# Kernel optimization log

Measured on AMD Instinct MI355X. Metric: run time of the kernel, lower is better.

## Reference

```python
import jax, jax.numpy as jnp
import numpy as np

N_NODES = 50000
N_EDGES = 800000
IN_CH = 64
HID_CH = 128
LAT_CH = 64
N_GRAPHS = 64
U_DIM = 32


def setup_inputs() -> dict:
    key = jax.random.key(0)
    ks = jax.random.split(key, 12)
    x = jax.random.normal(ks[0], (N_NODES, IN_CH), dtype=jnp.float32)
    edge_index = jax.random.randint(ks[1], (2, N_EDGES), 0, N_NODES, dtype=jnp.int64)
    edge_attr = jax.random.normal(ks[2], (N_EDGES, 8), dtype=jnp.float32)  # unused by NodeModel
    u = jax.random.normal(ks[3], (N_GRAPHS, U_DIM), dtype=jnp.float32)
    batch = jnp.sort(jax.random.randint(ks[4], (N_NODES,), 0, N_GRAPHS, dtype=jnp.int64))
    s = 0.02
    W1 = jax.random.normal(ks[5], (2 * IN_CH, HID_CH), dtype=jnp.float32) * s
    b1 = jnp.zeros((HID_CH,), dtype=jnp.float32)
    W2 = jax.random.normal(ks[6], (HID_CH, HID_CH), dtype=jnp.float32) * s
    b2 = jnp.zeros((HID_CH,), dtype=jnp.float32)
    W3 = jax.random.normal(ks[7], (HID_CH, LAT_CH), dtype=jnp.float32) * s
    b3 = jnp.zeros((LAT_CH,), dtype=jnp.float32)
    return {"x": x, "edge_index": edge_index, "edge_attr": edge_attr, "u": u,
            "batch": batch, "W1": W1, "b1": b1, "W2": W2, "b2": b2, "W3": W3, "b3": b3}


def reference(x, edge_index, edge_attr, u, batch, W1, b1, W2, b2, W3, b3):
    row, col = edge_index[0], edge_index[1]
    # gather endpoints -> [E, 2*in_ch]
    h = jnp.concatenate([x[row], x[col]], axis=1)
    # 3-layer MLP on edges
    h = jax.nn.relu(h @ W1 + b1)
    h = jax.nn.relu(h @ W2 + b2)
    h = h @ W3 + b3  # [E, latent]
    # scatter reductions over destination node (col)
    cnt = jax.ops.segment_sum(jnp.ones((h.shape[0],), h.dtype), col, num_segments=N_NODES)
    mean = jax.ops.segment_sum(h, col, num_segments=N_NODES) / jnp.maximum(cnt, 1.0)[:, None]
    mx = jax.ops.segment_max(h, col, num_segments=N_NODES)
    mn = jax.ops.segment_min(h, col, num_segments=N_NODES)
    nonempty = (cnt > 0)[:, None]
    mx = jnp.where(nonempty, mx, 0.0)  # torch_scatter returns 0 for empty segments
    mn = jnp.where(nonempty, mn, 0.0)
    return jnp.concatenate([x, mean, mx, mn, u[batch]], axis=1)
```

## Files before the change

kernel.cpp:

```cpp
#include <hip/hip_runtime.h>

#define E_EDGES 800000
#define NN 50000
#define OUT_STRIDE 288

typedef __bf16 bf16;
typedef bf16 bf16x8 __attribute__((ext_vector_type(8)));
typedef float floatx4 __attribute__((ext_vector_type(4)));
typedef float floatx2 __attribute__((ext_vector_type(2)));
typedef unsigned short ushort8v __attribute__((ext_vector_type(8)));

__device__ __forceinline__ unsigned short f2bf(float f){
    return __builtin_bit_cast(unsigned short, (bf16)f);
}
__device__ __forceinline__ unsigned pack2bf(float a, float b){
    unsigned short lo = __builtin_bit_cast(unsigned short, (bf16)a);
    unsigned short hi = __builtin_bit_cast(unsigned short, (bf16)b);
    return (unsigned)lo | ((unsigned)hi << 16);
}
__device__ __forceinline__ float bf2f(unsigned short h){
    return __uint_as_float((unsigned)h << 16);
}
__device__ __forceinline__ unsigned encf(float f){
    unsigned u = __float_as_uint(f);
    return (u & 0x80000000u) ? ~u : (u | 0x80000000u);
}
__device__ __forceinline__ float decf(unsigned u){
    return __uint_as_float((u & 0x80000000u) ? (u ^ 0x80000000u) : ~u);
}
__device__ __forceinline__ floatx4 mfma16(ushort8v a, ushort8v b, floatx4 c){
    return __builtin_amdgcn_mfma_f32_16x16x32_bf16(
        __builtin_bit_cast(bf16x8, a), __builtin_bit_cast(bf16x8, b), c, 0, 0, 0);
}
__device__ __forceinline__ void flush_run(float* out, int node, float s, float mx, float mn, int lane){
    float* sp = out + (long)node * OUT_STRIDE + 64;
    atomicAdd(sp + lane, s);
    atomicMax((unsigned*)sp + 64 + lane, encf(mx));
    atomicMin((unsigned*)sp + 128 + lane, encf(mn));
}
__device__ __forceinline__ ushort8v combine_relu_pq(ushort8v p, uint2 q){
    floatx2 q01 = __builtin_amdgcn_cvt_pk_f32_fp8((int)q.x, false);
    floatx2 q23 = __builtin_amdgcn_cvt_pk_f32_fp8((int)q.x, true);
    floatx2 q45 = __builtin_amdgcn_cvt_pk_f32_fp8((int)q.y, false);
    floatx2 q67 = __builtin_amdgcn_cvt_pk_f32_fp8((int)q.y, true);
    uint4 o;
    o.x = pack2bf(fmaxf(bf2f(p[0]) + q01[0], 0.f), fmaxf(bf2f(p[1]) + q01[1], 0.f));
    o.y = pack2bf(fmaxf(bf2f(p[2]) + q23[0], 0.f), fmaxf(bf2f(p[3]) + q23[1], 0.f));
    o.z = pack2bf(fmaxf(bf2f(p[4]) + q45[0], 0.f), fmaxf(bf2f(p[5]) + q45[1], 0.f));
    o.w = pack2bf(fmaxf(bf2f(p[6]) + q67[0], 0.f), fmaxf(bf2f(p[7]) + q67[1], 0.f));
    return __builtin_bit_cast(ushort8v, o);
}

#define INIT_N 2400000
#define PK_N   40960
#define SETUP_TOTAL (INIT_N + PK_N + E_EDGES)

__global__ void setup_kernel(const int* __restrict__ ei,
                             const float* __restrict__ W1, const float* __restrict__ W2,
                             const float* __restrict__ W3,
                             unsigned short* __restrict__ wp,
                             int* __restrict__ cnt, float* __restrict__ out)
{
    int i = blockIdx.x * blockDim.x + threadIdx.x;
    if (i < INIT_N) {
        int row = i / 48, q = i % 48;
        uint4 val = (q < 32) ? make_uint4(0u, 0u, 0u, 0u)
                             : make_uint4(~0u, ~0u, ~0u, ~0u);
        ((uint4*)out)[(long)row * 72 + 16 + q] = val;
        return;
    }
    i -= INIT_N;
    if (i < PK_N) {
        const float* W; int N; int idx;
        if (i < 16384)      { W = W1; N = 128; idx = i; }
        else if (i < 32768) { W = W2; N = 128; idx = i - 16384; }
        else                { W = W3; N = 64;  idx = i - 32768; }
        int j = idx & 7, lane = (idx >> 3) & 63, kc = (idx >> 9) & 3, nt = idx >> 11;
        wp[i] = f2bf(W[(kc * 32 + ((lane >> 4) & 3) * 8 + j) * N + nt * 16 + (lane & 15)]);
        return;
    }
    i -= PK_N;
    if (i < E_EDGES) atomicAdd(&cnt[ei[E_EDGES + i]], 1);
}

#define PQ_BLOCKS 391
__global__ __launch_bounds__(256, 4) void pq_kernel(
    const float* __restrict__ x, const unsigned short* __restrict__ wp,
    const float* __restrict__ b1, float* __restrict__ out, unsigned char* __restrict__ qb)
{
    const int tid = threadIdx.x, lane = tid & 63, w = tid >> 6;
    const int quad = lane >> 4, ln = lane & 15;
    const ushort8v* wpv = (const ushort8v*)wp;
    const int nbase = (blockIdx.x * 4 + w) * 32;
    const int n0 = nbase + ln, n1 = nbase + 16 + ln;
    const int n0c = min(n0, NN - 1), n1c = min(n1, NN - 1);

    ushort8v X0[2], X1[2];
#pragma unroll
    for (int c = 0; c < 2; c++){
        const float4* p0 = (const float4*)(x + (long)n0c * 64 + c * 32 + quad * 8);
        const float4* p1 = (const float4*)(x + (long)n1c * 64 + c * 32 + quad * 8);
        float4 a = p0[0], b = p0[1];
        float4 cc = p1[0], d = p1[1];
        uint4 u0, u1;
        u0.x = pack2bf(a.x, a.y);  u0.y = pack2bf(a.z, a.w);
        u0.z = pack2bf(b.x, b.y);  u0.w = pack2bf(b.z, b.w);
        u1.x = pack2bf(cc.x, cc.y); u1.y = pack2bf(cc.z, cc.w);
        u1.z = pack2bf(d.x, d.y);  u1.w = pack2bf(d.z, d.w);
        X0[c] = __builtin_bit_cast(ushort8v, u0);
        X1[c] = __builtin_bit_cast(ushort8v, u1);
    }
    unsigned char* ob = (unsigned char*)out;
#pragma unroll
    for (int nt = 0; nt < 8; nt++){
        floatx4 bini = *(const floatx4*)(b1 + nt * 16 + quad * 4);
        floatx4 z = {0.f, 0.f, 0.f, 0.f};
        floatx4 aP0 = bini, aP1 = bini, aQ0 = z, aQ1 = z;
        ushort8v Af0 = wpv[(nt * 4 + 0) * 64 + lane];
        ushort8v Af1 = wpv[(nt * 4 + 1) * 64 + lane];
        ushort8v Af2 = wpv[(nt * 4 + 2) * 64 + lane];
        ushort8v Af3 = wpv[(nt * 4 + 3) * 64 + lane];
        aP0 = mfma16(Af0, X0[0], aP0); aP0 = mfma16(Af1, X0[1], aP0);
        aP1 = mfma16(Af0, X1[0], aP1); aP1 = mfma16(Af1, X1[1], aP1);
        aQ0 = mfma16(Af2, X0[0], aQ0); aQ0 = mfma16(Af3, X0[1], aQ0);
        aQ1 = mfma16(Af2, X1[0], aQ1); aQ1 = mfma16(Af3, X1[1], aQ1);
        uint2 sP0, sP1;
        sP0.x = pack2bf(aP0[0], aP0[1]); sP0.y = pack2bf(aP0[2], aP0[3]);
        sP1.x = pack2bf(aP1[0], aP1[1]); sP1.y = pack2bf(aP1[2], aP1[3]);
        int bo = nt * 32 + quad * 8;
        int q0p = __builtin_amdgcn_cvt_pk_fp8_f32(aQ0[0], aQ0[1], 0, false);
        q0p     = __builtin_amdgcn_cvt_pk_fp8_f32(aQ0[2], aQ0[3], q0p, true);
        int q1p = __builtin_amdgcn_cvt_pk_fp8_f32(aQ1[0], aQ1[1], 0, false);
        q1p     = __builtin_amdgcn_cvt_pk_fp8_f32(aQ1[2], aQ1[3], q1p, true);
        int qo = nt * 16 + quad * 4;
        if (n0 < NN){
            *(uint2*)(ob + (long)n0 * 1152 + bo) = sP0;
            *(int*)(qb + (long)n0 * 128 + qo)    = q0p;
        }
        if (n1 < NN){
            *(uint2*)(ob + (long)n1 * 1152 + bo) = sP1;
            *(int*)(qb + (long)n1 * 128 + qo)    = q1p;
        }
    }
}

__global__ void scanA_kernel(const int* __restrict__ cnt, int* __restrict__ off,
                             int* __restrict__ bsum){
    __shared__ int s[256];
    int tid = threadIdx.x;
    int node = blockIdx.x * 196 + tid;
    int val = (tid < 196 && node < NN) ? cnt[node] : 0;
    s[tid] = val;
    __syncthreads();
    for (int d = 1; d < 256; d <<= 1){
        int t = (tid >= d) ? s[tid - d] : 0;
        __syncthreads();
        s[tid] += t;
        __syncthreads();
    }
    if (tid < 196 && node < NN) off[node] = s[tid] - val;
    if (tid == 255) bsum[blockIdx.x] = s[255];
}

__global__ void scanB_kernel(const int* __restrict__ bsum, int* __restrict__ bbase){
    __shared__ int s[256];
    int tid = threadIdx.x;
    int val = bsum[tid];
    s[tid] = val;
    __syncthreads();
    for (int d = 1; d < 256; d <<= 1){
        int t = (tid >= d) ? s[tid - d] : 0;
        __syncthreads();
        s[tid] += t;
        __syncthreads();
    }
    bbase[tid] = s[tid] - val;
}

__global__ void scatter_kernel(const int* __restrict__ ei, int* __restrict__ off,
                               const int* __restrict__ bbase, int2* __restrict__ enodes){
    int e = blockIdx.x * blockDim.x + threadIdx.x;
    if (e >= E_EDGES) return;
    int c = ei[E_EDGES + e], r = ei[e];
    int pos = atomicAdd(&off[c], 1) + bbase[c / 196];
    enodes[pos] = make_int2(r, c);
}

__global__ __launch_bounds__(256, 5) void edge_mlp_kernel(
    const int2* __restrict__ enodes, const unsigned short* __restrict__ wp,
    const unsigned char* __restrict__ qb,
    const float* __restrict__ b2, const float* __restrict__ b3,
    float* __restrict__ out)
{
    __shared__ __align__(16) unsigned char smem[4 * 4608];

    const int tid  = threadIdx.x;
    const int lane = tid & 63;
    const int w    = tid >> 6;
    const int quad = lane >> 4;
    const int ln   = lane & 15;
    unsigned short* wbuf = (unsigned short*)(smem + w * 4608);
    float* Tf = (float*)wbuf;
    const ushort8v* wpv = (const ushort8v*)wp;

    const int g = blockIdx.x * 4 + w;
    const int ebase = g * 32;
    int2 ed0 = enodes[ebase + ln];
    int2 ed1 = enodes[ebase + 16 + ln];
    const int cn0 = ed0.y, cn1 = ed1.y;

    const unsigned short* pqb = (const unsigned short*)out;
    ushort8v H0[4], H1[4];
#pragma unroll
    for (int kc = 0; kc < 4; kc++){
        const int o = kc * 32 + quad * 8;
        ushort8v p0 = *(const ushort8v*)(pqb + (long)ed0.x * 576 + o);
        ushort8v p1 = *(const ushort8v*)(pqb + (long)ed1.x * 576 + o);
        uint2 q0 = *(const uint2*)(qb + (long)ed0.y * 128 + o);
        uint2 q1 = *(const uint2*)(qb + (long)ed1.y * 128 + o);
        H0[kc] = combine_relu_pq(p0, q0);
        H1[kc] = combine_relu_pq(p1, q1);
    }

    ushort8v G0[4], G1[4];
#pragma unroll
    for (int hv = 0; hv < 2; hv++){
#pragma unroll
        for (int q2 = 0; q2 < 4; q2++){
            int nt = hv * 4 + q2;
            floatx4 bini = *(const floatx4*)(b2 + nt * 16 + quad * 4);
            floatx4 a0 = bini, a1 = bini;
#pragma unroll
            for (int kc = 0; kc < 4; kc++){
                ushort8v Af = wpv[2048 + (nt * 4 + kc) * 64 + lane];
                a0 = mfma16(Af, H0[kc], a0);
                a1 = mfma16(Af, H1[kc], a1);
            }
            uint2 p0, p1;
            p0.x = pack2bf(fmaxf(a0[0], 0.f), fmaxf(a0[1], 0.f));
            p0.y = pack2bf(fmaxf(a0[2], 0.f), fmaxf(a0[3], 0.f));
            p1.x = pack2bf(fmaxf(a1[0], 0.f), fmaxf(a1[1], 0.f));
            p1.y = pack2bf(fmaxf(a1[2], 0.f), fmaxf(a1[3], 0.f));
            int col = q2 * 16 + quad * 4;
            *(uint2*)(wbuf + ln * 72 + col)        = p0;
            *(uint2*)(wbuf + (16 + ln) * 72 + col) = p1;
        }
#pragma unroll
        for (int c = 0; c < 2; c++){
            G0[hv * 2 + c] = *(const ushort8v*)(wbuf + ln * 72 + c * 32 + quad * 8);
            G1[hv * 2 + c] = *(const ushort8v*)(wbuf + (16 + ln) * 72 + c * 32 + quad * 8);
        }
    }

#pragma unroll
    for (int hv = 0; hv < 2; hv++){
#pragma unroll
        for (int q3 = 0; q3 < 2; q3++){
            int nt = hv * 2 + q3;
            floatx4 bini = *(const floatx4*)(b3 + nt * 16 + quad * 4);
            floatx4 a0 = bini, a1 = bini;
#pragma unroll
            for (int kc = 0; kc < 4; kc++){
                ushort8v Af = wpv[4096 + (nt * 4 + kc) * 64 + lane];
                a0 = mfma16(Af, G0[kc], a0);
                a1 = mfma16(Af, G1[kc], a1);
            }
            int row = q3 * 16 + quad * 4;
#pragma unroll
            for (int r = 0; r < 4; r++){
                Tf[(row + r) * 36 + ln]      = a0[r];
                Tf[(row + r) * 36 + 16 + ln] = a1[r];
            }
        }
        if ((lane >> 5) == hv){
            float v[32];
#pragma unroll
            for (int jj = 0; jj < 8; jj++){
                floatx4 t = *(const floatx4*)(Tf + (lane & 31) * 36 + jj * 4);
                v[jj * 4 + 0] = t[0]; v[jj * 4 + 1] = t[1];
                v[jj * 4 + 2] = t[2]; v[jj * 4 + 3] = t[3];
            }
            int cur = __builtin_amdgcn_readlane(cn0, 0);
            float s = v[0], mx = v[0], mn = v[0];
#pragma unroll
            for (int j = 1; j < 32; j++){
                int nj = (j < 16) ? __builtin_amdgcn_readlane(cn0, j)
                                  : __builtin_amdgcn_readlane(cn1, j - 16);
                if (nj != cur){
                    flush_run(out, cur, s, mx, mn, lane);
                    cur = nj; s = v[j]; mx = v[j]; mn = v[j];
                } else {
                    s += v[j]; mx = fmaxf(mx, v[j]); mn = fminf(mn, v[j]);
                }
            }
            flush_run(out, cur, s, mx, mn, lane);
        }
    }
}

__global__ void finalize_kernel(const float* __restrict__ x, const float* __restrict__ u,
                                const int* __restrict__ batch, const int* __restrict__ cnt,
                                float* __restrict__ out)
{
    long i = (long)blockIdx.x * blockDim.x + threadIdx.x;
    if (i >= (long)NN * 72) return;
    int ndx = (int)(i / 72);
    int q   = (int)(i % 72);
    float4 res;
    if (q < 16) {
        res = ((const float4*)(x + (long)ndx * 64))[q];
    } else if (q < 32) {
        float4 sv = ((const float4*)out)[i];
        int k = cnt[ndx];
        float inv = 1.f / (float)(k > 0 ? k : 1);
        res.x = sv.x * inv; res.y = sv.y * inv; res.z = sv.z * inv; res.w = sv.w * inv;
    } else if (q < 64) {
        uint4 e = ((const uint4*)out)[i];
        bool ne = cnt[ndx] > 0;
        res.x = ne ? decf(e.x) : 0.f; res.y = ne ? decf(e.y) : 0.f;
        res.z = ne ? decf(e.z) : 0.f; res.w = ne ? decf(e.w) : 0.f;
    } else {
        res = ((const float4*)(u + (long)batch[ndx] * 32))[q - 64];
    }
    ((float4*)out)[i] = res;
}

extern "C" void kernel_launch(void* const* d_in, const int* in_sizes, int n_in,
                              void* d_out, int out_size, void* d_ws, size_t ws_size,
                              hipStream_t stream)
{
    const float* x     = (const float*)d_in[0];
    const int*   ei    = (const int*)d_in[1];
    const float* u     = (const float*)d_in[3];
    const int*   batch = (const int*)d_in[4];
    const float* W1    = (const float*)d_in[5];
    const float* b1    = (const float*)d_in[6];
    const float* W2    = (const float*)d_in[7];
    const float* b2    = (const float*)d_in[8];
    const float* W3    = (const float*)d_in[9];
    const float* b3    = (const float*)d_in[10];
    float* out = (float*)d_out;
    unsigned char* ws = (unsigned char*)d_ws;

    unsigned short* wp     = (unsigned short*)ws;
    int*            cnt    = (int*)(ws + 81920);
    int*            off    = (int*)(ws + 281920);
    int*            bsum   = (int*)(ws + 481920);
    int*            bbase  = (int*)(ws + 482944);
    int2*           enodes = (int2*)(ws + 483968);
    unsigned char*  qb     = (unsigned char*)(ws + 6883968);

    hipMemsetAsync(cnt, 0, 200000, stream);
    setup_kernel<<<(SETUP_TOTAL + 255) / 256, 256, 0, stream>>>(ei, W1, W2, W3, wp, cnt, out);
    pq_kernel<<<PQ_BLOCKS, 256, 0, stream>>>(x, wp, b1, out, qb);
    scanA_kernel<<<256, 256, 0, stream>>>(cnt, off, bsum);
    scanB_kernel<<<1, 256, 0, stream>>>(bsum, bbase);
    scatter_kernel<<<(E_EDGES + 255) / 256, 256, 0, stream>>>(ei, off, bbase, enodes);
    edge_mlp_kernel<<<6250, 256, 0, stream>>>(enodes, wp, qb, b2, b3, out);
    finalize_kernel<<<(int)(((long)NN * 72 + 255) / 256), 256, 0, stream>>>(x, u, batch, cnt, out);
}
```

Measured before the change: 363.9 us.

## Store P table in fp8, pack edge indices, restructure layer-3 reduction

The first-layer source-node projection P is now stored as fp8 in a separate 128-byte-per-node buffer instead of bf16 inside the output tensor, with a permuted layout so each lane loads its 32 bytes in two 16-byte reads. Edge endpoints are packed into one 32-bit word (16-bit row and column), which halves the size of the sorted edge list. The layer-3 result is staged in LDS as bf16, and all 64 lanes each reduce one channel over both 16-edge halves, instead of two half-wave passes through a float staging buffer. Occupancy bounds rise from 5 to 8 blocks. The aim is less gather bandwidth and fewer serial reduction passes, at the cost of extra fp8 and bf16 rounding error, and the 16-bit packing only holds while node indices fit in 16 bits.

Result: no change. 361.9 us (-0.6%).

```diff
diff --git a/kernel.cpp b/kernel.cpp
--- a/kernel.cpp
+++ b/kernel.cpp
@@ -18,9 +18,6 @@
     unsigned short hi = __builtin_bit_cast(unsigned short, (bf16)b);
     return (unsigned)lo | ((unsigned)hi << 16);
 }
-__device__ __forceinline__ float bf2f(unsigned short h){
-    return __uint_as_float((unsigned)h << 16);
-}
 __device__ __forceinline__ unsigned encf(float f){
     unsigned u = __float_as_uint(f);
     return (u & 0x80000000u) ? ~u : (u | 0x80000000u);
@@ -38,16 +35,21 @@
     atomicMax((unsigned*)sp + 64 + lane, encf(mx));
     atomicMin((unsigned*)sp + 128 + lane, encf(mn));
 }
-__device__ __forceinline__ ushort8v combine_relu_pq(ushort8v p, uint2 q){
+__device__ __forceinline__ ushort8v combine_relu_fp8(uint2 p, uint2 q){
+    floatx2 p01 = __builtin_amdgcn_cvt_pk_f32_fp8((int)p.x, false);
+    floatx2 p23 = __builtin_amdgcn_cvt_pk_f32_fp8((int)p.x, true);
+    floatx2 p45 = __builtin_amdgcn_cvt_pk_f32_fp8((int)p.y, false);
+    floatx2 p67 = __builtin_amdgcn_cvt_pk_f32_fp8((int)p.y, true);
     floatx2 q01 = __builtin_amdgcn_cvt_pk_f32_fp8((int)q.x, false);
     floatx2 q23 = __builtin_amdgcn_cvt_pk_f32_fp8((int)q.x, true);
     floatx2 q45 = __builtin_amdgcn_cvt_pk_f32_fp8((int)q.y, false);
     floatx2 q67 = __builtin_amdgcn_cvt_pk_f32_fp8((int)q.y, true);
+    floatx2 s01 = p01 + q01, s23 = p23 + q23, s45 = p45 + q45, s67 = p67 + q67;
     uint4 o;
-    o.x = pack2bf(fmaxf(bf2f(p[0]) + q01[0], 0.f), fmaxf(bf2f(p[1]) + q01[1], 0.f));
-    o.y = pack2bf(fmaxf(bf2f(p[2]) + q23[0], 0.f), fmaxf(bf2f(p[3]) + q23[1], 0.f));
-    o.z = pack2bf(fmaxf(bf2f(p[4]) + q45[0], 0.f), fmaxf(bf2f(p[5]) + q45[1], 0.f));
-    o.w = pack2bf(fmaxf(bf2f(p[6]) + q67[0], 0.f), fmaxf(bf2f(p[7]) + q67[1], 0.f));
+    o.x = pack2bf(fmaxf(s01[0], 0.f), fmaxf(s01[1], 0.f));
+    o.y = pack2bf(fmaxf(s23[0], 0.f), fmaxf(s23[1], 0.f));
+    o.z = pack2bf(fmaxf(s45[0], 0.f), fmaxf(s45[1], 0.f));
+    o.w = pack2bf(fmaxf(s67[0], 0.f), fmaxf(s67[1], 0.f));
     return __builtin_bit_cast(ushort8v, o);
 }
 
@@ -86,7 +88,8 @@
 #define PQ_BLOCKS 391
 __global__ __launch_bounds__(256, 4) void pq_kernel(
     const float* __restrict__ x, const unsigned short* __restrict__ wp,
-    const float* __restrict__ b1, float* __restrict__ out, unsigned char* __restrict__ qb)
+    const float* __restrict__ b1,
+    unsigned char* __restrict__ pb, unsigned char* __restrict__ qb)
 {
     const int tid = threadIdx.x, lane = tid & 63, w = tid >> 6;
     const int quad = lane >> 4, ln = lane & 15;
@@ -110,7 +113,6 @@
         X0[c] = __builtin_bit_cast(ushort8v, u0);
         X1[c] = __builtin_bit_cast(ushort8v, u1);
     }
-    unsigned char* ob = (unsigned char*)out;
 #pragma unroll
     for (int nt = 0; nt < 8; nt++){
         floatx4 bini = *(const floatx4*)(b1 + nt * 16 + quad * 4);
@@ -124,22 +126,22 @@
         aP1 = mfma16(Af0, X1[0], aP1); aP1 = mfma16(Af1, X1[1], aP1);
         aQ0 = mfma16(Af2, X0[0], aQ0); aQ0 = mfma16(Af3, X0[1], aQ0);
         aQ1 = mfma16(Af2, X1[0], aQ1); aQ1 = mfma16(Af3, X1[1], aQ1);
-        uint2 sP0, sP1;
-        sP0.x = pack2bf(aP0[0], aP0[1]); sP0.y = pack2bf(aP0[2], aP0[3]);
-        sP1.x = pack2bf(aP1[0], aP1[1]); sP1.y = pack2bf(aP1[2], aP1[3]);
-        int bo = nt * 32 + quad * 8;
+        int p0p = __builtin_amdgcn_cvt_pk_fp8_f32(aP0[0], aP0[1], 0, false);
+        p0p     = __builtin_amdgcn_cvt_pk_fp8_f32(aP0[2], aP0[3], p0p, true);
+        int p1p = __builtin_amdgcn_cvt_pk_fp8_f32(aP1[0], aP1[1], 0, false);
+        p1p     = __builtin_amdgcn_cvt_pk_fp8_f32(aP1[2], aP1[3], p1p, true);
         int q0p = __builtin_amdgcn_cvt_pk_fp8_f32(aQ0[0], aQ0[1], 0, false);
         q0p     = __builtin_amdgcn_cvt_pk_fp8_f32(aQ0[2], aQ0[3], q0p, true);
         int q1p = __builtin_amdgcn_cvt_pk_fp8_f32(aQ1[0], aQ1[1], 0, false);
         q1p     = __builtin_amdgcn_cvt_pk_fp8_f32(aQ1[2], aQ1[3], q1p, true);
-        int qo = nt * 16 + quad * 4;
+        int g0 = ((nt & 1) * 2 + (quad >> 1)) * 32 + (nt >> 1) * 8 + (quad & 1) * 4;
         if (n0 < NN){
-            *(uint2*)(ob + (long)n0 * 1152 + bo) = sP0;
-            *(int*)(qb + (long)n0 * 128 + qo)    = q0p;
+            *(int*)(pb + (long)n0 * 128 + g0) = p0p;
+            *(int*)(qb + (long)n0 * 128 + g0) = q0p;
         }
         if (n1 < NN){
-            *(uint2*)(ob + (long)n1 * 1152 + bo) = sP1;
-            *(int*)(qb + (long)n1 * 128 + qo)    = q1p;
+            *(int*)(pb + (long)n1 * 128 + g0) = p1p;
+            *(int*)(qb + (long)n1 * 128 + g0) = q1p;
         }
     }
 }
@@ -178,48 +180,56 @@
 }
 
 __global__ void scatter_kernel(const int* __restrict__ ei, int* __restrict__ off,
-                               const int* __restrict__ bbase, int2* __restrict__ enodes){
+                               const int* __restrict__ bbase, unsigned* __restrict__ enodes){
     int e = blockIdx.x * blockDim.x + threadIdx.x;
     if (e >= E_EDGES) return;
     int c = ei[E_EDGES + e], r = ei[e];
     int pos = atomicAdd(&off[c], 1) + bbase[c / 196];
-    enodes[pos] = make_int2(r, c);
-}
-
-__global__ __launch_bounds__(256, 5) void edge_mlp_kernel(
-    const int2* __restrict__ enodes, const unsigned short* __restrict__ wp,
-    const unsigned char* __restrict__ qb,
+    enodes[pos] = (unsigned)r | ((unsigned)c << 16);
+}
+
+__global__ __launch_bounds__(256, 8) void edge_mlp_kernel(
+    const unsigned* __restrict__ enodes, const unsigned short* __restrict__ wp,
+    const unsigned char* __restrict__ pb, const unsigned char* __restrict__ qb,
     const float* __restrict__ b2, const float* __restrict__ b3,
     float* __restrict__ out)
 {
-    __shared__ __align__(16) unsigned char smem[4 * 4608];
+    __shared__ __align__(16) unsigned char smem[4 * 4864];
 
     const int tid  = threadIdx.x;
     const int lane = tid & 63;
     const int w    = tid >> 6;
     const int quad = lane >> 4;
     const int ln   = lane & 15;
-    unsigned short* wbuf = (unsigned short*)(smem + w * 4608);
-    float* Tf = (float*)wbuf;
+    unsigned short* wbuf = (unsigned short*)(smem + w * 4864);
     const ushort8v* wpv = (const ushort8v*)wp;
 
     const int g = blockIdx.x * 4 + w;
     const int ebase = g * 32;
-    int2 ed0 = enodes[ebase + ln];
-    int2 ed1 = enodes[ebase + 16 + ln];
-    const int cn0 = ed0.y, cn1 = ed1.y;
-
-    const unsigned short* pqb = (const unsigned short*)out;
+    unsigned e0 = enodes[ebase + ln];
+    unsigned e1 = enodes[ebase + 16 + ln];
+    const int r0 = (int)(e0 & 0xFFFFu), cn0 = (int)(e0 >> 16);
+    const int r1 = (int)(e1 & 0xFFFFu), cn1 = (int)(e1 >> 16);
+
     ushort8v H0[4], H1[4];
-#pragma unroll
-    for (int kc = 0; kc < 4; kc++){
-        const int o = kc * 32 + quad * 8;
-        ushort8v p0 = *(const ushort8v*)(pqb + (long)ed0.x * 576 + o);
-        ushort8v p1 = *(const ushort8v*)(pqb + (long)ed1.x * 576 + o);
-        uint2 q0 = *(const uint2*)(qb + (long)ed0.y * 128 + o);
-        uint2 q1 = *(const uint2*)(qb + (long)ed1.y * 128 + o);
-        H0[kc] = combine_relu_pq(p0, q0);
-        H1[kc] = combine_relu_pq(p1, q1);
+    {
+        const long po = (long)quad * 32;
+        uint4 pA = *(const uint4*)(pb + (long)r0  * 128 + po);
+        uint4 pB = *(const uint4*)(pb + (long)r0  * 128 + po + 16);
+        uint4 qA = *(const uint4*)(qb + (long)cn0 * 128 + po);
+        uint4 qB = *(const uint4*)(qb + (long)cn0 * 128 + po + 16);
+        uint4 rA = *(const uint4*)(pb + (long)r1  * 128 + po);
+        uint4 rB = *(const uint4*)(pb + (long)r1  * 128 + po + 16);
+        uint4 sA = *(const uint4*)(qb + (long)cn1 * 128 + po);
+        uint4 sB = *(const uint4*)(qb + (long)cn1 * 128 + po + 16);
+        H0[0] = combine_relu_fp8(make_uint2(pA.x, pA.y), make_uint2(qA.x, qA.y));
+        H0[1] = combine_relu_fp8(make_uint2(pA.z, pA.w), make_uint2(qA.z, qA.w));
+        H0[2] = combine_relu_fp8(make_uint2(pB.x, pB.y), make_uint2(qB.x, qB.y));
+        H0[3] = combine_relu_fp8(make_uint2(pB.z, pB.w), make_uint2(qB.z, qB.w));
+        H1[0] = combine_relu_fp8(make_uint2(rA.x, rA.y), make_uint2(sA.x, sA.y));
+        H1[1] = combine_relu_fp8(make_uint2(rA.z, rA.w), make_uint2(sA.z, sA.w));
+        H1[2] = combine_relu_fp8(make_uint2(rB.x, rB.y), make_uint2(sB.x, sB.y));
+        H1[3] = combine_relu_fp8(make_uint2(rB.z, rB.w), make_uint2(sB.z, sB.w));
     }
 
     ushort8v G0[4], G1[4];
@@ -253,49 +263,56 @@
     }
 
 #pragma unroll
-    for (int hv = 0; hv < 2; hv++){
-#pragma unroll
-        for (int q3 = 0; q3 < 2; q3++){
-            int nt = hv * 2 + q3;
-            floatx4 bini = *(const floatx4*)(b3 + nt * 16 + quad * 4);
-            floatx4 a0 = bini, a1 = bini;
-#pragma unroll
-            for (int kc = 0; kc < 4; kc++){
-                ushort8v Af = wpv[4096 + (nt * 4 + kc) * 64 + lane];
-                a0 = mfma16(Af, G0[kc], a0);
-                a1 = mfma16(Af, G1[kc], a1);
-            }
-            int row = q3 * 16 + quad * 4;
-#pragma unroll
-            for (int r = 0; r < 4; r++){
-                Tf[(row + r) * 36 + ln]      = a0[r];
-                Tf[(row + r) * 36 + 16 + ln] = a1[r];
-            }
-        }
-        if ((lane >> 5) == hv){
-            float v[32];
-#pragma unroll
-            for (int jj = 0; jj < 8; jj++){
-                floatx4 t = *(const floatx4*)(Tf + (lane & 31) * 36 + jj * 4);
-                v[jj * 4 + 0] = t[0]; v[jj * 4 + 1] = t[1];
-                v[jj * 4 + 2] = t[2]; v[jj * 4 + 3] = t[3];
-            }
-            int cur = __builtin_amdgcn_readlane(cn0, 0);
-            float s = v[0], mx = v[0], mn = v[0];
-#pragma unroll
-            for (int j = 1; j < 32; j++){
-                int nj = (j < 16) ? __builtin_amdgcn_readlane(cn0, j)
-                                  : __builtin_amdgcn_readlane(cn1, j - 16);
-                if (nj != cur){
-                    flush_run(out, cur, s, mx, mn, lane);
-                    cur = nj; s = v[j]; mx = v[j]; mn = v[j];
-                } else {
-                    s += v[j]; mx = fmaxf(mx, v[j]); mn = fminf(mn, v[j]);
-                }
-            }
-            flush_run(out, cur, s, mx, mn, lane);
-        }
-    }
+    for (int nt = 0; nt < 4; nt++){
+        floatx4 bini = *(const floatx4*)(b3 + nt * 16 + quad * 4);
+        floatx4 a0 = bini, a1 = bini;
+#pragma unroll
+        for (int kc = 0; kc < 4; kc++){
+            ushort8v Af = wpv[4096 + (nt * 4 + kc) * 64 + lane];
+            a0 = mfma16(Af, G0[kc], a0);
+            a1 = mfma16(Af, G1[kc], a1);
+        }
+        int och = nt * 16 + quad * 4;
+#pragma unroll
+        for (int r = 0; r < 4; r++){
+            wbuf[(och + r) * 38 + ln]      = f2bf(a0[r]);
+            wbuf[(och + r) * 38 + 16 + ln] = f2bf(a1[r]);
+        }
+    }
+
+    float v[32];
+#pragma unroll
+    for (int t = 0; t < 8; t++){
+        unsigned a = *(const unsigned*)(wbuf + lane * 38 + t * 4);
+        unsigned b = *(const unsigned*)(wbuf + lane * 38 + t * 4 + 2);
+        v[t * 4 + 0] = __uint_as_float(a << 16);
+        v[t * 4 + 1] = __uint_as_float(a & 0xFFFF0000u);
+        v[t * 4 + 2] = __uint_as_float(b << 16);
+        v[t * 4 + 3] = __uint_as_float(b & 0xFFFF0000u);
+    }
+    int curA = __builtin_amdgcn_readlane(cn0, 0);
+    int curB = __builtin_amdgcn_readlane(cn1, 0);
+    float sA = v[0],  mxA = v[0],  mnA = v[0];
+    float sB = v[16], mxB = v[16], mnB = v[16];
+#pragma unroll
+    for (int j = 1; j < 16; j++){
+        int njA = __builtin_amdgcn_readlane(cn0, j);
+        int njB = __builtin_amdgcn_readlane(cn1, j);
+        if (njA != curA){
+            flush_run(out, curA, sA, mxA, mnA, lane);
+            curA = njA; sA = v[j]; mxA = v[j]; mnA = v[j];
+        } else {
+            sA += v[j]; mxA = fmaxf(mxA, v[j]); mnA = fminf(mnA, v[j]);
+        }
+        if (njB != curB){
+            flush_run(out, curB, sB, mxB, mnB, lane);
+            curB = njB; sB = v[16 + j]; mxB = v[16 + j]; mnB = v[16 + j];
+        } else {
+            sB += v[16 + j]; mxB = fmaxf(mxB, v[16 + j]); mnB = fminf(mnB, v[16 + j]);
+        }
+    }
+    flush_run(out, curA, sA, mxA, mnA, lane);
+    flush_run(out, curB, sB, mxB, mnB, lane);
 }
 
 __global__ void finalize_kernel(const float* __restrict__ x, const float* __restrict__ u,
@@ -347,15 +364,16 @@
     int*            off    = (int*)(ws + 281920);
     int*            bsum   = (int*)(ws + 481920);
     int*            bbase  = (int*)(ws + 482944);
-    int2*           enodes = (int2*)(ws + 483968);
-    unsigned char*  qb     = (unsigned char*)(ws + 6883968);
+    unsigned*       enodes = (unsigned*)(ws + 483968);
+    unsigned char*  pb     = (unsigned char*)(ws + 3683968);
+    unsigned char*  qb     = (unsigned char*)(ws + 10083968);
 
     hipMemsetAsync(cnt, 0, 200000, stream);
     setup_kernel<<<(SETUP_TOTAL + 255) / 256, 256, 0, stream>>>(ei, W1, W2, W3, wp, cnt, out);
-    pq_kernel<<<PQ_BLOCKS, 256, 0, stream>>>(x, wp, b1, out, qb);
+    pq_kernel<<<PQ_BLOCKS, 256, 0, stream>>>(x, wp, b1, pb, qb);
     scanA_kernel<<<256, 256, 0, stream>>>(cnt, off, bsum);
     scanB_kernel<<<1, 256, 0, stream>>>(bsum, bbase);
     scatter_kernel<<<(E_EDGES + 255) / 256, 256, 0, stream>>>(ei, off, bbase, enodes);
-    edge_mlp_kernel<<<6250, 256, 0, stream>>>(enodes, wp, qb, b2, b3, out);
+    edge_mlp_kernel<<<6250, 256, 0, stream>>>(enodes, wp, pb, qb, b2, b3, out);
     finalize_kernel<<<(int)(((long)NN * 72 + 255) / 256), 256, 0, stream>>>(x, u, batch, cnt, out);
 }
```
